# Optimization experiments

Measured on AMD Instinct MI355X. Metric: run time of the kernel, lower is better.

The kernel has to match this reference:

```python
import jax, jax.numpy as jnp
import numpy as np


def hard_sigmoid(x):
    # Keras/Theano hard_sigmoid: clip(0.2*x + 0.5, 0, 1)
    return jnp.clip(0.2 * x + 0.5, 0.0, 1.0)


def _lstm_scan(x, Wi, Ui, bi, Wf, Uf, bf, Wc, Uc, bc, Wo, Uo, bo):
    # x: [B, T, D]. Precompute input-to-gate projections as big GEMMs -> [T, B, H]
    xi = jnp.einsum('btd,dh->tbh', x, Wi) + bi
    xf = jnp.einsum('btd,dh->tbh', x, Wf) + bf
    xc = jnp.einsum('btd,dh->tbh', x, Wc) + bc
    xo = jnp.einsum('btd,dh->tbh', x, Wo) + bo

    B = x.shape[0]
    H = Ui.shape[0]
    h0 = jnp.zeros((B, H), dtype=x.dtype)
    c0 = jnp.zeros((B, H), dtype=x.dtype)

    def step(carry, gates):
        h, c = carry
        gi, gf, go, gc = gates
        i_t = hard_sigmoid(gi + h @ Ui)
        f_t = hard_sigmoid(gf + h @ Uf)
        o_t = hard_sigmoid(go + h @ Uo)
        g_t = jnp.tanh(gc + h @ Uc)
        c_t = f_t * c + i_t * g_t
        h_t = o_t * jnp.tanh(c_t)
        return (h_t, c_t), h_t

    _, hs = jax.lax.scan(step, (h0, c0), (xi, xf, xo, xc))  # hs: [T, B, H]
    return hs.transpose(1, 0, 2)  # [B, T, H]


def _bidir_lstm(x,
                W_i, U_i, b_i, W_f, U_f, b_f, W_c, U_c, b_c, W_o, U_o, b_o,
                Wb_i, Ub_i, bb_i, Wb_f, Ub_f, bb_f, Wb_c, Ub_c, bb_c, Wb_o, Ub_o, bb_o):
    forward = _lstm_scan(x, W_i, U_i, b_i, W_f, U_f, b_f, W_c, U_c, b_c, W_o, U_o, b_o)
    # Theano scan(go_backwards=True) iterates the reversed sequence and stacks
    # outputs in iteration order WITHOUT re-reversing; replicate by flipping x
    # in time and not flipping the scan output back.
    backward = _lstm_scan(x[:, ::-1, :], Wb_i, Ub_i, bb_i, Wb_f, Ub_f, bb_f,
                          Wb_c, Ub_c, bb_c, Wb_o, Ub_o, bb_o)
    # output_mode == 'sum', return_sequences == True
    return forward + backward  # [B, T, H]


def setup_inputs() -> dict:
    B, T, D, H = 32, 512, 512, 512
    key = jax.random.key(0)
    keys = jax.random.split(key, 17)
    x = jax.random.normal(keys[0], (B, T, D), dtype=jnp.float32)
    s_w = 1.0 / np.sqrt(D)   # glorot-ish for input weights
    s_u = 1.0 / np.sqrt(H)   # orthogonal-ish scale for recurrent weights
    names = ['W_i', 'W_f', 'W_c', 'W_o', 'Wb_i', 'Wb_f', 'Wb_c', 'Wb_o']
    unames = ['U_i', 'U_f', 'U_c', 'U_o', 'Ub_i', 'Ub_f', 'Ub_c', 'Ub_o']
    inp = {'x': x}
    for j, n in enumerate(names):
        inp[n] = jax.random.normal(keys[1 + j], (D, H), dtype=jnp.float32) * s_w
    for j, n in enumerate(unames):
        inp[n] = jax.random.normal(keys[9 + j], (H, H), dtype=jnp.float32) * s_u
    for n in ['b_i', 'b_f', 'b_c', 'b_o', 'bb_i', 'bb_f', 'bb_c', 'bb_o']:
        inp[n] = jnp.zeros((H,), dtype=jnp.float32)
    return inp


def reference(x,
              W_i, U_i, b_i, W_f, U_f, b_f, W_c, U_c, b_c, W_o, U_o, b_o,
              Wb_i, Ub_i, bb_i, Wb_f, Ub_f, bb_f, Wb_c, Ub_c, bb_c, Wb_o, Ub_o, bb_o):
    return _bidir_lstm(x,
                       W_i, U_i, b_i, W_f, U_f, b_f, W_c, U_c, b_c, W_o, U_o, b_o,
                       Wb_i, Ub_i, bb_i, Wb_f, Ub_f, bb_f, Wb_c, Ub_c, bb_c,
                       Wb_o, Ub_o, bb_o)
```

## Files before the change

### kernel.cpp

```cpp
#include <hip/hip_runtime.h>

typedef _Float16 half8 __attribute__((ext_vector_type(8)));
typedef float f32x4 __attribute__((ext_vector_type(4)));

#define TT 512
#define HH 512

#define OFF_HPK   16777216
#define OFF_FLAGS 50331648
#define OFF_UPK   50339840
#define OFF_WPK   54534144

struct BiasPtrs { const float* b[8]; };

struct PackParams {
  const float* U[8];
  const float* W[8];
  _Float16* Upk;
  _Float16* Wpk;
};

__global__ void convert_x_kernel(const float* __restrict__ x, _Float16* __restrict__ x16) {
  const size_t i = ((size_t)blockIdx.x * blockDim.x + threadIdx.x) * 8;
  float4 v0 = *(const float4*)(x + i);
  float4 v1 = *(const float4*)(x + i + 4);
  half8 h;
  h[0] = (_Float16)v0.x; h[1] = (_Float16)v0.y; h[2] = (_Float16)v0.z; h[3] = (_Float16)v0.w;
  h[4] = (_Float16)v1.x; h[5] = (_Float16)v1.y; h[6] = (_Float16)v1.z; h[7] = (_Float16)v1.w;
  *(half8*)(x16 + i) = h;
}

__global__ void pack_frags_kernel(PackParams p) {
  const unsigned n = blockIdx.x * 256 + threadIdx.x;
  const unsigned o = n & 2097151u;
  const int sel = n >> 21;
  const int jj = o & 7, l = (o >> 3) & 63, kt = (o >> 9) & 15;
  const int ct = (o >> 13) & 1, j = (o >> 14) & 63, d = (o >> 20) & 1;
  const int r15 = l & 15, kg = l >> 4;
  const int g = r15 & 3;
  const int u = j * 8 + ct * 4 + (r15 >> 2);
  const int k = kt * 32 + kg * 8 + jj;
  const float* M = sel ? p.W[4 * d + g] : p.U[4 * d + g];
  _Float16* dst = sel ? p.Wpk : p.Upk;
  dst[o] = (_Float16)M[k * HH + u];
}

__global__ void zero_flags_kernel(int* __restrict__ p) {
  __hip_atomic_store(p + blockIdx.x * 256 + threadIdx.x, 0,
                     __ATOMIC_RELAXED, __HIP_MEMORY_SCOPE_AGENT);
}

__device__ __forceinline__ float hsig(float x) {
  return fminf(fmaxf(fmaf(x, 0.2f, 0.5f), 0.0f), 1.0f);
}

__device__ __forceinline__ float fast_tanh(float x) {
  const float e = __expf(2.0f * x);
  return fmaf(-2.0f, __builtin_amdgcn_rcpf(e + 1.0f), 1.0f);
}

__global__ __launch_bounds__(256, 1) void lstm_scan_kernel(
    const _Float16* __restrict__ x16,
    _Float16* __restrict__ h_pk,
    int* __restrict__ flags,
    const _Float16* __restrict__ Upk,
    const _Float16* __restrict__ Wpk,
    BiasPtrs bp) {
  const int tid = threadIdx.x;
  const int bid = blockIdx.x;
  const int d   = bid >> 6;
  const int j   = bid & 63;
  const int w   = tid >> 6;
  const int l   = tid & 63;
  const int r15 = l & 15;
  const int kg  = l >> 4;
  const int rt  = w & 1;
  const int ct  = w >> 1;
  const int arow = rt * 16 + r15;

  __shared__ __align__(16) half8 ulds[2 * 16 * 64];
  __shared__ __align__(16) half8 wlds[2 * 16 * 64];
  __shared__ __align__(16) float zlds[32 * 36];
  __shared__ __align__(16) unsigned short hlds[256];

  {
    const half8* ub = (const half8*)Upk;
    const half8* wb = (const half8*)Wpk;
    const int base = (((d * 64 + j) * 2 + ct) * 16) * 64 + l;
    if (rt == 0) {
#pragma unroll
      for (int kt = 0; kt < 16; ++kt) {
        ulds[(ct * 16 + kt) * 64 + l] = ub[base + kt * 64];
        wlds[(ct * 16 + kt) * 64 + l] = wb[base + kt * 64];
      }
    }
  }

  const int b_e  = tid >> 3;
  const int uu_e = tid & 7;
  const int u_e  = j * 8 + uu_e;
  const int slot_e = (uu_e >> 2) * 16 + (uu_e & 3) * 4;
  f32x4 biasv;
#pragma unroll
  for (int g = 0; g < 4; ++g) biasv[g] = bp.b[4 * d + g][u_e];

  __syncthreads();

  float c = 0.0f;

  for (int s = 0; s < TT; ++s) {
    const int t = d ? (TT - 1 - s) : s;

    half8 xa[16];
    {
      const half8* xb = (const half8*)(x16 + ((size_t)arow * TT + t) * HH);
#pragma unroll
      for (int kt = 0; kt < 16; ++kt) xa[kt] = xb[kt * 4 + kg];
    }
    __builtin_amdgcn_sched_barrier(0);

    if (s > 0) {
      if (tid < 64) {
        const int* fl = flags + ((d * 8 + ((s - 1) & 7)) << 6) + tid;
        while (__hip_atomic_load(fl, __ATOMIC_RELAXED, __HIP_MEMORY_SCOPE_AGENT) < s) {
          __builtin_amdgcn_s_sleep(1);
        }
      }
      __syncthreads();
    }
    __builtin_amdgcn_sched_barrier(0);

    half8 ha[16];
    if (s > 0) {
      const half8* hb = (const half8*)(h_pk + (size_t)(d * TT + (s - 1)) * 16384);
#pragma unroll
      for (int kt = 0; kt < 16; ++kt) ha[kt] = hb[(kt * 4 + kg) * 32 + arow];
    }
    __builtin_amdgcn_sched_barrier(0);

    f32x4 acc0 = {0,0,0,0}, acc1 = {0,0,0,0}, acc2 = {0,0,0,0}, acc3 = {0,0,0,0};
#pragma unroll
    for (int kt = 0; kt < 16; ++kt) {
      const half8 wk = wlds[(ct * 16 + kt) * 64 + l];
      if ((kt & 3) == 0)      acc0 = __builtin_amdgcn_mfma_f32_16x16x32_f16(xa[kt], wk, acc0, 0, 0, 0);
      else if ((kt & 3) == 1) acc1 = __builtin_amdgcn_mfma_f32_16x16x32_f16(xa[kt], wk, acc1, 0, 0, 0);
      else if ((kt & 3) == 2) acc2 = __builtin_amdgcn_mfma_f32_16x16x32_f16(xa[kt], wk, acc2, 0, 0, 0);
      else                    acc3 = __builtin_amdgcn_mfma_f32_16x16x32_f16(xa[kt], wk, acc3, 0, 0, 0);
    }
    __builtin_amdgcn_sched_barrier(0);

    if (s > 0) {
#pragma unroll
      for (int kt = 0; kt < 16; ++kt) {
        const half8 uk = ulds[(ct * 16 + kt) * 64 + l];
        if ((kt & 3) == 0)      acc0 = __builtin_amdgcn_mfma_f32_16x16x32_f16(ha[kt], uk, acc0, 0, 0, 0);
        else if ((kt & 3) == 1) acc1 = __builtin_amdgcn_mfma_f32_16x16x32_f16(ha[kt], uk, acc1, 0, 0, 0);
        else if ((kt & 3) == 2) acc2 = __builtin_amdgcn_mfma_f32_16x16x32_f16(ha[kt], uk, acc2, 0, 0, 0);
        else                    acc3 = __builtin_amdgcn_mfma_f32_16x16x32_f16(ha[kt], uk, acc3, 0, 0, 0);
      }
    }
    const f32x4 z = (acc0 + acc1) + (acc2 + acc3);

#pragma unroll
    for (int i = 0; i < 4; ++i)
      zlds[(rt * 16 + kg * 4 + i) * 36 + ct * 16 + r15] = z[i];
    __syncthreads();

    f32x4 pre = *(const f32x4*)&zlds[(size_t)b_e * 36 + slot_e] + biasv;
    const float ig = hsig(pre[0]);
    const float fg = hsig(pre[1]);
    const float gg = fast_tanh(pre[2]);
    const float og = hsig(pre[3]);
    c = fg * c + ig * gg;
    const float h = og * fast_tanh(c);

    hlds[tid] = __builtin_bit_cast(unsigned short, (_Float16)h);
    __syncthreads();

    if (tid < 64) {
      const unsigned long long v = ((const unsigned long long*)hlds)[tid];
      unsigned long long* dst = (unsigned long long*)h_pk +
                                ((size_t)(d * TT + s) * 64 + j) * 64 + tid;
      __hip_atomic_store(dst, v, __ATOMIC_RELAXED, __HIP_MEMORY_SCOPE_AGENT);
      asm volatile("s_waitcnt vmcnt(0)" ::: "memory");
      if (tid == 0)
        __hip_atomic_store(flags + ((d * 8 + (s & 7)) << 6) + j, s + 1,
                           __ATOMIC_RELAXED, __HIP_MEMORY_SCOPE_AGENT);
    }
  }
}

__global__ void sum_out_kernel(const _Float16* __restrict__ h_pk, float* __restrict__ out) {
  const unsigned idx = blockIdx.x * 256 + threadIdx.x;
  const int j = idx & 63;
  const int t = (idx >> 6) & 511;
  const int b = idx >> 15;
  half8 hf = ((const half8*)h_pk)[((size_t)t * 64 + j) * 32 + b];
  half8 hg = ((const half8*)h_pk)[((size_t)(TT + t) * 64 + j) * 32 + b];
  float* o = out + (((size_t)b * TT + t) * HH + j * 8);
  float4 r0, r1;
  r0.x = (float)hf[0] + (float)hg[0]; r0.y = (float)hf[1] + (float)hg[1];
  r0.z = (float)hf[2] + (float)hg[2]; r0.w = (float)hf[3] + (float)hg[3];
  r1.x = (float)hf[4] + (float)hg[4]; r1.y = (float)hf[5] + (float)hg[5];
  r1.z = (float)hf[6] + (float)hg[6]; r1.w = (float)hf[7] + (float)hg[7];
  *(float4*)o = r0;
  *(float4*)(o + 4) = r1;
}

extern "C" void kernel_launch(void* const* d_in, const int* in_sizes, int n_in,
                              void* d_out, int out_size, void* d_ws, size_t ws_size,
                              hipStream_t stream) {
  (void)in_sizes; (void)n_in; (void)out_size; (void)ws_size;
  char* ws = (char*)d_ws;
  _Float16* x16   = (_Float16*)ws;
  _Float16* h_pk  = (_Float16*)(ws + OFF_HPK);
  int*      flags = (int*)(ws + OFF_FLAGS);
  _Float16* Upk   = (_Float16*)(ws + OFF_UPK);
  _Float16* Wpk   = (_Float16*)(ws + OFF_WPK);

  convert_x_kernel<<<4096, 256, 0, stream>>>((const float*)d_in[0], x16);

  PackParams pp;
  for (int g = 0; g < 8; ++g) {
    pp.W[g] = (const float*)d_in[1 + g];
    pp.U[g] = (const float*)d_in[9 + g];
  }
  pp.Upk = Upk; pp.Wpk = Wpk;
  pack_frags_kernel<<<16384, 256, 0, stream>>>(pp);

  zero_flags_kernel<<<4, 256, 0, stream>>>(flags);

  BiasPtrs bp;
  for (int g = 0; g < 8; ++g) bp.b[g] = (const float*)d_in[17 + g];

  void* args[] = { (void*)&x16, (void*)&h_pk, (void*)&flags,
                   (void*)&Upk, (void*)&Wpk, (void*)&bp };
  hipLaunchCooperativeKernel((const void*)lstm_scan_kernel, dim3(128), dim3(256),
                             args, 0, stream);

  sum_out_kernel<<<4096, 256, 0, stream>>>(h_pk, (float*)d_out);
}
```

Baseline: 1.773 ms.

## Halve scan workgroups to 64 with 512 threads each, 16 hidden units per block

Repartitions the cooperative recurrent kernel from 128 blocks of 256 threads (8 hidden units each) to 64 blocks of 512 threads (16 hidden units each). Weight fragment packing, LDS buffers, flag layout and the h output layout are changed to match, keeping the same global h_pk format. The aim is to cut the number of blocks taking part in each per-timestep cross-block flag barrier, at the cost of more work per block on the serial critical path and a larger LDS footprint.

```diff
diff --git a/kernel.cpp b/kernel.cpp
--- a/kernel.cpp
+++ b/kernel.cpp
@@ -35,10 +35,10 @@
   const unsigned o = n & 2097151u;
   const int sel = n >> 21;
   const int jj = o & 7, l = (o >> 3) & 63, kt = (o >> 9) & 15;
-  const int ct = (o >> 13) & 1, j = (o >> 14) & 63, d = (o >> 20) & 1;
+  const int ct = (o >> 13) & 3, slot = (o >> 15) & 31, d = (o >> 20) & 1;
   const int r15 = l & 15, kg = l >> 4;
   const int g = r15 & 3;
-  const int u = j * 8 + ct * 4 + (r15 >> 2);
+  const int u = slot * 16 + ct * 4 + (r15 >> 2);
   const int k = kt * 32 + kg * 8 + jj;
   const float* M = sel ? p.W[4 * d + g] : p.U[4 * d + g];
   _Float16* dst = sel ? p.Wpk : p.Upk;
@@ -59,50 +59,51 @@
   return fmaf(-2.0f, __builtin_amdgcn_rcpf(e + 1.0f), 1.0f);
 }
 
-__global__ __launch_bounds__(256, 1) void lstm_scan_kernel(
+__global__ __launch_bounds__(512, 1) void lstm_scan_kernel(
     const _Float16* __restrict__ x16,
     _Float16* __restrict__ h_pk,
     int* __restrict__ flags,
     const _Float16* __restrict__ Upk,
     const _Float16* __restrict__ Wpk,
     BiasPtrs bp) {
-  const int tid = threadIdx.x;
-  const int bid = blockIdx.x;
-  const int d   = bid >> 6;
-  const int j   = bid & 63;
-  const int w   = tid >> 6;
-  const int l   = tid & 63;
-  const int r15 = l & 15;
-  const int kg  = l >> 4;
-  const int rt  = w & 1;
-  const int ct  = w >> 1;
+  const int tid  = threadIdx.x;
+  const int bid  = blockIdx.x;
+  const int d    = bid >> 5;
+  const int slot = bid & 31;
+  const int w    = tid >> 6;
+  const int l    = tid & 63;
+  const int r15  = l & 15;
+  const int kg   = l >> 4;
+  const int rt   = w & 1;
+  const int ct   = w >> 1;
   const int arow = rt * 16 + r15;
 
-  __shared__ __align__(16) half8 ulds[2 * 16 * 64];
-  __shared__ __align__(16) half8 wlds[2 * 16 * 64];
-  __shared__ __align__(16) float zlds[32 * 36];
-  __shared__ __align__(16) unsigned short hlds[256];
+  __shared__ __align__(16) half8 ulds[4 * 16 * 64];
+  __shared__ __align__(16) half8 wlds[4 * 16 * 64];
+  __shared__ __align__(16) float zlds[32 * 68];
+  __shared__ __align__(16) unsigned short hlds[512];
 
   {
-    const half8* ub = (const half8*)Upk;
-    const half8* wb = (const half8*)Wpk;
-    const int base = (((d * 64 + j) * 2 + ct) * 16) * 64 + l;
+    const int fb = (((d * 32 + slot) * 4 + ct) * 16) * 64 + l;
     if (rt == 0) {
-#pragma unroll
-      for (int kt = 0; kt < 16; ++kt) {
-        ulds[(ct * 16 + kt) * 64 + l] = ub[base + kt * 64];
-        wlds[(ct * 16 + kt) * 64 + l] = wb[base + kt * 64];
-      }
+      const half8* ub = (const half8*)Upk;
+#pragma unroll
+      for (int kt = 0; kt < 16; ++kt)
+        ulds[(ct * 16 + kt) * 64 + l] = ub[fb + kt * 64];
+    } else {
+      const half8* wb = (const half8*)Wpk;
+#pragma unroll
+      for (int kt = 0; kt < 16; ++kt)
+        wlds[(ct * 16 + kt) * 64 + l] = wb[fb + kt * 64];
     }
   }
 
-  const int b_e  = tid >> 3;
-  const int uu_e = tid & 7;
-  const int u_e  = j * 8 + uu_e;
-  const int slot_e = (uu_e >> 2) * 16 + (uu_e & 3) * 4;
+  const int b_e = tid >> 4;
+  const int uu  = tid & 15;
+  const int se0 = (uu >> 2) * 16 + (uu & 3) * 4;
   f32x4 biasv;
 #pragma unroll
-  for (int g = 0; g < 4; ++g) biasv[g] = bp.b[4 * d + g][u_e];
+  for (int g = 0; g < 4; ++g) biasv[g] = bp.b[4 * d + g][slot * 16 + uu];
 
   __syncthreads();
 
@@ -120,8 +121,8 @@
     __builtin_amdgcn_sched_barrier(0);
 
     if (s > 0) {
-      if (tid < 64) {
-        const int* fl = flags + ((d * 8 + ((s - 1) & 7)) << 6) + tid;
+      if (tid < 32) {
+        const int* fl = flags + d * 256 + (((s - 1) & 7) << 5) + tid;
         while (__hip_atomic_load(fl, __ATOMIC_RELAXED, __HIP_MEMORY_SCOPE_AGENT) < s) {
           __builtin_amdgcn_s_sleep(1);
         }
@@ -163,28 +164,30 @@
 
 #pragma unroll
     for (int i = 0; i < 4; ++i)
-      zlds[(rt * 16 + kg * 4 + i) * 36 + ct * 16 + r15] = z[i];
+      zlds[(rt * 16 + kg * 4 + i) * 68 + ct * 16 + r15] = z[i];
     __syncthreads();
 
-    f32x4 pre = *(const f32x4*)&zlds[(size_t)b_e * 36 + slot_e] + biasv;
+    f32x4 pre = *(const f32x4*)&zlds[(size_t)b_e * 68 + se0] + biasv;
     const float ig = hsig(pre[0]);
     const float fg = hsig(pre[1]);
     const float gg = fast_tanh(pre[2]);
     const float og = hsig(pre[3]);
     c = fg * c + ig * gg;
     const float h = og * fast_tanh(c);
-
-    hlds[tid] = __builtin_bit_cast(unsigned short, (_Float16)h);
+    hlds[((uu >> 3) << 8) + b_e * 8 + (uu & 7)] =
+        __builtin_bit_cast(unsigned short, (_Float16)h);
     __syncthreads();
 
     if (tid < 64) {
-      const unsigned long long v = ((const unsigned long long*)hlds)[tid];
+      const unsigned long long v0 = ((const unsigned long long*)hlds)[2 * tid];
+      const unsigned long long v1 = ((const unsigned long long*)hlds)[2 * tid + 1];
       unsigned long long* dst = (unsigned long long*)h_pk +
-                                ((size_t)(d * TT + s) * 64 + j) * 64 + tid;
-      __hip_atomic_store(dst, v, __ATOMIC_RELAXED, __HIP_MEMORY_SCOPE_AGENT);
+                                ((size_t)(d * TT + s) * 4096) + slot * 128 + 2 * tid;
+      __hip_atomic_store(dst,     v0, __ATOMIC_RELAXED, __HIP_MEMORY_SCOPE_AGENT);
+      __hip_atomic_store(dst + 1, v1, __ATOMIC_RELAXED, __HIP_MEMORY_SCOPE_AGENT);
       asm volatile("s_waitcnt vmcnt(0)" ::: "memory");
       if (tid == 0)
-        __hip_atomic_store(flags + ((d * 8 + (s & 7)) << 6) + j, s + 1,
+        __hip_atomic_store(flags + d * 256 + ((s & 7) << 5) + slot, s + 1,
                            __ATOMIC_RELAXED, __HIP_MEMORY_SCOPE_AGENT);
     }
   }
@@ -228,14 +231,14 @@
   pp.Upk = Upk; pp.Wpk = Wpk;
   pack_frags_kernel<<<16384, 256, 0, stream>>>(pp);
 
-  zero_flags_kernel<<<4, 256, 0, stream>>>(flags);
+  zero_flags_kernel<<<2, 256, 0, stream>>>(flags);
 
   BiasPtrs bp;
   for (int g = 0; g < 8; ++g) bp.b[g] = (const float*)d_in[17 + g];
 
   void* args[] = { (void*)&x16, (void*)&h_pk, (void*)&flags,
                    (void*)&Upk, (void*)&Wpk, (void*)&bp };
-  hipLaunchCooperativeKernel((const void*)lstm_scan_kernel, dim3(128), dim3(256),
+  hipLaunchCooperativeKernel((const void*)lstm_scan_kernel, dim3(64), dim3(512),
                              args, 0, stream);
 
   sum_out_kernel<<<4096, 256, 0, stream>>>(h_pk, (float*)d_out);
```

Result: slower. 2.792 ms (+57.5%).
